# Performance work log

Hardware: AMD Instinct MI355X
Metric: run time of the kernel (lower is better)

Reference implementation:

```python
import jax, jax.numpy as jnp
import numpy as np

B = 65536
N_CHILDREN = 512
HIDDEN = 64


def setup_inputs() -> dict:
    key = jax.random.key(0)
    k1, k2, k3, k4, k5, k6, k7 = jax.random.split(key, 7)
    x_cpm = jax.random.normal(k1, (B, N_CHILDREN), dtype=jnp.float32)
    x_cons = jax.random.normal(k2, (B, 1), dtype=jnp.float32)
    # per-child capacities, strictly positive (used as divisor)
    cap = jax.random.uniform(k3, (1, N_CHILDREN), dtype=jnp.float32) + 0.5
    # small MLP params (torch Linear layout: W is (out, in))
    s1 = 1.0 / np.sqrt(N_CHILDREN + 1)
    s2 = 1.0 / np.sqrt(HIDDEN)
    W1 = jax.random.normal(k4, (HIDDEN, N_CHILDREN + 1), dtype=jnp.float32) * s1
    b1 = jax.random.normal(k5, (HIDDEN,), dtype=jnp.float32) * s1
    W2 = jax.random.normal(k6, (N_CHILDREN, HIDDEN), dtype=jnp.float32) * s2
    b2 = jax.random.normal(k7, (N_CHILDREN,), dtype=jnp.float32) * s2
    return {"x_cpm": x_cpm, "x_cons": x_cons, "cap": cap,
            "W1": W1, "b1": b1, "W2": W2, "b2": b2}


def reference(x_cpm, x_cons, cap, W1, b1, W2, b2):
    cap_sum = jnp.sum(cap)  # scalar Cap_sum
    # epsilon: (B, 1) residual of the aggregate constraint
    epsilon = (x_cons * cap_sum - jnp.sum(x_cpm * cap, axis=1, keepdims=True)) / cap_sum
    concat_input = jnp.concatenate([x_cpm, epsilon], axis=1)  # (B, n_l + 1)
    h1 = jax.nn.relu(concat_input @ W1.T + b1)                # (B, 64)
    z = h1 @ W2.T + b2                                        # (B, n_l)
    # symmetric activation: tanh then row-normalize by the signed sum
    signed = jnp.tanh(z)
    h = signed / jnp.sum(signed, axis=1, keepdims=True)
    # reconcile
    x_c = (x_cpm * cap + h * epsilon * cap_sum) / cap
    return x_c
```

## Files before the change

kernel.cpp:

```cpp
#include <hip/hip_runtime.h>
#include <hip/hip_fp16.h>
#include <math.h>

#define THREADS 256
#define RPB 32
#define NBLK (65536 / RPB)

#define WS_W1    0
#define WS_W1_CH 3072
#define WS_W2    (16 * WS_W1_CH)
#define WS_W2_CH 8192
#define WS_W1L   (WS_W2 + 4 * WS_W2_CH)

#define OFF_W    0
#define SZ_W     32768
#define W1BUF_B  12288
#define OFF_T    (OFF_W + SZ_W)
#define SZ_T     (RPB * 516 * 2)
#define OFF_H1   (OFF_T + SZ_T)
#define SZ_H1    (RPB * 68 * 4)
#define OFF_CI   (OFF_H1 + SZ_H1)
#define SZ_CI    2048
#define OFF_EPS  (OFF_CI + SZ_CI)
#define OFF_EPSC (OFF_EPS + 128)
#define OFF_RS   (OFF_EPSC + 128)
#define SMEM_BYTES (OFF_RS + 128)

__device__ __forceinline__ float fast_tanh(float z) {
    float e = __expf(2.0f * z);
    return fmaf(-2.0f, __builtin_amdgcn_rcpf(e + 1.0f), 1.0f);
}

__global__ __launch_bounds__(256) void prep_kernel(
    const float* __restrict__ W1, const float* __restrict__ W2,
    float* __restrict__ ws)
{
    int tid = blockIdx.x * 256 + threadIdx.x;
    {
        int it = tid >> 11;
        int rem = tid & 2047;
        int jj = rem >> 6, c = rem & 63;
        ws[WS_W1 + it * WS_W1_CH + jj * 68 + c] = W1[c * 513 + it * 32 + jj];
    }
    {
        int j = tid & 3, kf4 = (tid >> 2) & 15, n = (tid >> 6) & 127, ch = tid >> 13;
        int swz = kf4 ^ ((9 * (n >> 2) + (n & 3)) & 15);
        ws[WS_W2 + ch * WS_W2_CH + n * 64 + swz * 4 + j] = W2[tid];
    }
    if (tid < 64) ws[WS_W1L + tid] = W1[tid * 513 + 512];
}

__global__ __launch_bounds__(THREADS, 2) void fused_rgu(
    const float* __restrict__ x, const float* __restrict__ xcons,
    const float* __restrict__ cap, const float* __restrict__ b1,
    const float* __restrict__ b2, const float* __restrict__ ws,
    float* __restrict__ out)
{
    extern __shared__ __align__(16) char smem[];
    float*          s_w    = (float*)(smem + OFF_W);
    unsigned short* s_t    = (unsigned short*)(smem + OFF_T);
    float*          s_h1   = (float*)(smem + OFF_H1);
    float*          s_ci   = (float*)(smem + OFF_CI);
    float*          s_eps  = (float*)(smem + OFF_EPS);
    float*          s_epsC = (float*)(smem + OFF_EPSC);
    float*          s_rs   = (float*)(smem + OFF_RS);

    const int t    = threadIdx.x;
    const int lane = t & 63;
    const int wv   = t >> 6;
    const long r0  = (long)blockIdx.x * RPB;

    {
        const float4* src = (const float4*)(ws + WS_W1);
        float4* dst = (float4*)(smem + OFF_W);
        dst[t] = src[t]; dst[t + 256] = src[t + 256]; dst[t + 512] = src[t + 512];
    }

    float4 capA = *(const float4*)(cap + 4 * lane);
    float4 capB = *(const float4*)(cap + 256 + 4 * lane);
    {
        float c0 = cap[t], c1 = cap[t + 256];
        s_ci[t] = 1.0f / c0; s_ci[t + 256] = 1.0f / c1;
    }
    float capSum;
    {
        float p = capA.x + capA.y + capA.z + capA.w
                + capB.x + capB.y + capB.z + capB.w;
        #pragma unroll
        for (int m = 1; m < 64; m <<= 1) p += __shfl_xor(p, m, 64);
        capSum = p;
    }
    const float invCapSum = 1.0f / capSum;

    #pragma unroll
    for (int rr = 0; rr < 8; ++rr) {
        int r = wv * 8 + rr;
        const float* xr = x + (r0 + r) * 512;
        float4 xA = *(const float4*)(xr + 4 * lane);
        float4 xB = *(const float4*)(xr + 256 + 4 * lane);
        float d = fmaf(xA.x, capA.x, fmaf(xA.y, capA.y,
                  fmaf(xA.z, capA.z, fmaf(xA.w, capA.w,
                  fmaf(xB.x, capB.x, fmaf(xB.y, capB.y,
                  fmaf(xB.z, capB.z, xB.w * capB.w)))))));
        #pragma unroll
        for (int m = 1; m < 64; m <<= 1) d += __shfl_xor(d, m, 64);
        if (lane == 0) {
            float epsC = fmaf(xcons[r0 + r], capSum, -d);
            s_epsC[r] = epsC;
            s_eps[r]  = epsC * invCapSum;
        }
    }
    __syncthreads();

    const int rg = t >> 4;
    const int cg = t & 15;
    float acc0[4] = {0.f, 0.f, 0.f, 0.f};
    float acc1[4] = {0.f, 0.f, 0.f, 0.f};
    {
        const float* xg0 = x + (r0 + 2 * rg) * 512;
        const float* xg1 = xg0 + 512;
        for (int it = 0; it < 16; ++it) {
            const int b = it & 1;
            if (it < 15) {
                const float4* src = (const float4*)(ws + WS_W1 + (it + 1) * WS_W1_CH);
                float4* dst = (float4*)(smem + OFF_W + (b ^ 1) * W1BUF_B);
                dst[t] = src[t]; dst[t + 256] = src[t + 256]; dst[t + 512] = src[t + 512];
            }
            const float* w = (const float*)(smem + OFF_W + b * W1BUF_B);
            const int k0 = it * 32;
            #pragma unroll
            for (int j4 = 0; j4 < 8; ++j4) {
                float4 xv0 = *(const float4*)(xg0 + k0 + j4 * 4);
                float4 xv1 = *(const float4*)(xg1 + k0 + j4 * 4);
                const float* wb = &w[(j4 * 4) * 68 + 4 * cg];
                float wr[4][4];
                #pragma unroll
                for (int dj = 0; dj < 4; ++dj) {
                    float4 w4 = *(const float4*)(wb + dj * 68);
                    wr[dj][0] = w4.x; wr[dj][1] = w4.y; wr[dj][2] = w4.z; wr[dj][3] = w4.w;
                }
                #pragma unroll
                for (int m = 0; m < 4; ++m) {
                    acc0[m] = fmaf(xv0.x, wr[0][m], fmaf(xv0.y, wr[1][m],
                              fmaf(xv0.z, wr[2][m], fmaf(xv0.w, wr[3][m], acc0[m]))));
                    acc1[m] = fmaf(xv1.x, wr[0][m], fmaf(xv1.y, wr[1][m],
                              fmaf(xv1.z, wr[2][m], fmaf(xv1.w, wr[3][m], acc1[m]))));
                }
            }
            __syncthreads();
        }
        float4 b1v = *(const float4*)(b1 + 4 * cg);
        float4 wl  = *(const float4*)(ws + WS_W1L + 4 * cg);
        #pragma unroll
        for (int i = 0; i < 2; ++i) {
            float e = s_eps[2 * rg + i];
            const float* a = i ? acc1 : acc0;
            float4 h;
            h.x = fmaxf(a[0] + fmaf(e, wl.x, b1v.x), 0.f);
            h.y = fmaxf(a[1] + fmaf(e, wl.y, b1v.y), 0.f);
            h.z = fmaxf(a[2] + fmaf(e, wl.z, b1v.z), 0.f);
            h.w = fmaxf(a[3] + fmaf(e, wl.w, b1v.w), 0.f);
            *(float4*)&s_h1[(2 * rg + i) * 68 + 4 * cg] = h;
        }
    }

    const int ng  = t & 31;
    const int rg2 = t >> 5;
    float rsum[4] = {0.f, 0.f, 0.f, 0.f};
    for (int ch = 0; ch < 4; ++ch) {
        __syncthreads();
        {
            const float4* src = (const float4*)(ws + WS_W2 + ch * WS_W2_CH);
            float4* dst = (float4*)(smem + OFF_W);
            #pragma unroll
            for (int e8 = 0; e8 < 8; ++e8) dst[e8 * 256 + t] = src[e8 * 256 + t];
        }
        __syncthreads();
        const int n0 = ch * 128;
        float4 b2v = *(const float4*)(b2 + n0 + 4 * ng);
        float za[4][4];
        #pragma unroll
        for (int i = 0; i < 4; ++i) {
            za[i][0] = b2v.x; za[i][1] = b2v.y; za[i][2] = b2v.z; za[i][3] = b2v.w;
        }
        #pragma unroll
        for (int kf4 = 0; kf4 < 16; ++kf4) {
            float hr[4][4];
            #pragma unroll
            for (int i = 0; i < 4; ++i) {
                float4 h = *(const float4*)&s_h1[(rg2 * 4 + i) * 68 + kf4 * 4];
                hr[i][0] = h.x; hr[i][1] = h.y; hr[i][2] = h.z; hr[i][3] = h.w;
            }
            float wr2[4][4];
            #pragma unroll
            for (int m = 0; m < 4; ++m) {
                int nl = 4 * ng + m;
                int swz = kf4 ^ ((9 * ng + m) & 15);
                float4 w = *(const float4*)&s_w[nl * 64 + swz * 4];
                wr2[m][0] = w.x; wr2[m][1] = w.y; wr2[m][2] = w.z; wr2[m][3] = w.w;
            }
            #pragma unroll
            for (int i = 0; i < 4; ++i)
                #pragma unroll
                for (int m = 0; m < 4; ++m)
                    za[i][m] = fmaf(hr[i][0], wr2[m][0], fmaf(hr[i][1], wr2[m][1],
                               fmaf(hr[i][2], wr2[m][2], fmaf(hr[i][3], wr2[m][3], za[i][m]))));
        }
        #pragma unroll
        for (int i = 0; i < 4; ++i) {
            int r = rg2 * 4 + i;
            float t0 = fast_tanh(za[i][0]);
            float t1 = fast_tanh(za[i][1]);
            float t2 = fast_tanh(za[i][2]);
            float t3 = fast_tanh(za[i][3]);
            rsum[i] += (t0 + t1) + (t2 + t3);
            ushort4 tv4;
            tv4.x = __half_as_ushort(__float2half(t0));
            tv4.y = __half_as_ushort(__float2half(t1));
            tv4.z = __half_as_ushort(__float2half(t2));
            tv4.w = __half_as_ushort(__float2half(t3));
            *(ushort4*)&s_t[r * 516 + n0 + 4 * ng] = tv4;
        }
    }
    #pragma unroll
    for (int i = 0; i < 4; ++i) {
        float s = rsum[i];
        #pragma unroll
        for (int msk = 1; msk < 32; msk <<= 1) s += __shfl_xor(s, msk, 64);
        if (ng == 0) {
            int r = rg2 * 4 + i;
            s_rs[r] = s_epsC[r] / s;
        }
    }
    __syncthreads();

    {
        const int rr  = t >> 7;
        const int col = (t & 127) * 4;
        #pragma unroll 4
        for (int q = 0; q < 16; ++q) {
            int r = q * 2 + rr;
            float rs = s_rs[r];
            float4 xv = *(const float4*)(x + (r0 + r) * 512 + col);
            ushort4 tv4 = *(const ushort4*)&s_t[r * 516 + col];
            float4 ci = *(const float4*)&s_ci[col];
            float4 o;
            o.x = fmaf(__half2float(__ushort_as_half(tv4.x)), rs * ci.x, xv.x);
            o.y = fmaf(__half2float(__ushort_as_half(tv4.y)), rs * ci.y, xv.y);
            o.z = fmaf(__half2float(__ushort_as_half(tv4.z)), rs * ci.z, xv.z);
            o.w = fmaf(__half2float(__ushort_as_half(tv4.w)), rs * ci.w, xv.w);
            *(float4*)(out + (r0 + r) * 512 + col) = o;
        }
    }
}

extern "C" void kernel_launch(void* const* d_in, const int* in_sizes, int n_in,
                              void* d_out, int out_size, void* d_ws, size_t ws_size,
                              hipStream_t stream) {
    const float* x     = (const float*)d_in[0];
    const float* xcons = (const float*)d_in[1];
    const float* cap   = (const float*)d_in[2];
    const float* W1    = (const float*)d_in[3];
    const float* b1    = (const float*)d_in[4];
    const float* W2    = (const float*)d_in[5];
    const float* b2    = (const float*)d_in[6];
    float* out         = (float*)d_out;
    float* ws          = (float*)d_ws;

    (void)in_sizes; (void)n_in; (void)out_size; (void)ws_size;

    prep_kernel<<<128, 256, 0, stream>>>(W1, W2, ws);

    hipFuncSetAttribute((const void*)fused_rgu,
                        hipFuncAttributeMaxDynamicSharedMemorySize, SMEM_BYTES);
    fused_rgu<<<NBLK, THREADS, SMEM_BYTES, stream>>>(
        x, xcons, cap, b1, b2, ws, out);
}
```

Baseline: 444.3 us.

## Keep tanh results in registers instead of LDS and raise occupancy

Packed fp16 tanh outputs now stay in per-thread registers (32 uints) rather than being staged through a shared-memory tile, and the row-sum reciprocal is used directly after the wave shuffle reduction. This removes the s_t and s_rs LDS buffers along with a barrier and the LDS round trip. The smaller LDS footprint plus launch bounds raised to 3 blocks per CU aim for higher occupancy. The cost is more register pressure under the tighter register cap, and the final x/out accesses now follow the GEMM thread mapping (32 threads per row, 16B each, four 512B segments per row) instead of the previous fully contiguous row sweep.

```diff
diff --git a/kernel.cpp b/kernel.cpp
--- a/kernel.cpp
+++ b/kernel.cpp
@@ -15,16 +15,13 @@
 #define OFF_W    0
 #define SZ_W     32768
 #define W1BUF_B  12288
-#define OFF_T    (OFF_W + SZ_W)
-#define SZ_T     (RPB * 516 * 2)
-#define OFF_H1   (OFF_T + SZ_T)
+#define OFF_H1   (OFF_W + SZ_W)
 #define SZ_H1    (RPB * 68 * 4)
 #define OFF_CI   (OFF_H1 + SZ_H1)
 #define SZ_CI    2048
 #define OFF_EPS  (OFF_CI + SZ_CI)
 #define OFF_EPSC (OFF_EPS + 128)
-#define OFF_RS   (OFF_EPSC + 128)
-#define SMEM_BYTES (OFF_RS + 128)
+#define SMEM_BYTES (OFF_EPSC + 128)
 
 __device__ __forceinline__ float fast_tanh(float z) {
     float e = __expf(2.0f * z);
@@ -50,7 +47,7 @@
     if (tid < 64) ws[WS_W1L + tid] = W1[tid * 513 + 512];
 }
 
-__global__ __launch_bounds__(THREADS, 2) void fused_rgu(
+__global__ __launch_bounds__(THREADS, 3) void fused_rgu(
     const float* __restrict__ x, const float* __restrict__ xcons,
     const float* __restrict__ cap, const float* __restrict__ b1,
     const float* __restrict__ b2, const float* __restrict__ ws,
@@ -58,12 +55,10 @@
 {
     extern __shared__ __align__(16) char smem[];
     float*          s_w    = (float*)(smem + OFF_W);
-    unsigned short* s_t    = (unsigned short*)(smem + OFF_T);
     float*          s_h1   = (float*)(smem + OFF_H1);
     float*          s_ci   = (float*)(smem + OFF_CI);
     float*          s_eps  = (float*)(smem + OFF_EPS);
     float*          s_epsC = (float*)(smem + OFF_EPSC);
-    float*          s_rs   = (float*)(smem + OFF_RS);
 
     const int t    = threadIdx.x;
     const int lane = t & 63;
@@ -167,6 +162,8 @@
     const int ng  = t & 31;
     const int rg2 = t >> 5;
     float rsum[4] = {0.f, 0.f, 0.f, 0.f};
+    unsigned tp[4][4][2];
+    #pragma unroll
     for (int ch = 0; ch < 4; ++ch) {
         __syncthreads();
         {
@@ -208,48 +205,46 @@
         }
         #pragma unroll
         for (int i = 0; i < 4; ++i) {
-            int r = rg2 * 4 + i;
             float t0 = fast_tanh(za[i][0]);
             float t1 = fast_tanh(za[i][1]);
             float t2 = fast_tanh(za[i][2]);
             float t3 = fast_tanh(za[i][3]);
             rsum[i] += (t0 + t1) + (t2 + t3);
-            ushort4 tv4;
-            tv4.x = __half_as_ushort(__float2half(t0));
-            tv4.y = __half_as_ushort(__float2half(t1));
-            tv4.z = __half_as_ushort(__float2half(t2));
-            tv4.w = __half_as_ushort(__float2half(t3));
-            *(ushort4*)&s_t[r * 516 + n0 + 4 * ng] = tv4;
-        }
-    }
+            __half2 h01 = __floats2half2_rn(t0, t1);
+            __half2 h23 = __floats2half2_rn(t2, t3);
+            tp[ch][i][0] = *(unsigned*)&h01;
+            tp[ch][i][1] = *(unsigned*)&h23;
+        }
+    }
+
+    float rs[4];
     #pragma unroll
     for (int i = 0; i < 4; ++i) {
         float s = rsum[i];
         #pragma unroll
         for (int msk = 1; msk < 32; msk <<= 1) s += __shfl_xor(s, msk, 64);
-        if (ng == 0) {
-            int r = rg2 * 4 + i;
-            s_rs[r] = s_epsC[r] / s;
-        }
-    }
-    __syncthreads();
-
-    {
-        const int rr  = t >> 7;
-        const int col = (t & 127) * 4;
-        #pragma unroll 4
-        for (int q = 0; q < 16; ++q) {
-            int r = q * 2 + rr;
-            float rs = s_rs[r];
-            float4 xv = *(const float4*)(x + (r0 + r) * 512 + col);
-            ushort4 tv4 = *(const ushort4*)&s_t[r * 516 + col];
-            float4 ci = *(const float4*)&s_ci[col];
+        rs[i] = s_epsC[rg2 * 4 + i] / s;
+    }
+
+    #pragma unroll
+    for (int ch = 0; ch < 4; ++ch) {
+        const int c = ch * 128 + 4 * ng;
+        float4 ci = *(const float4*)&s_ci[c];
+        #pragma unroll
+        for (int i = 0; i < 4; ++i) {
+            const int r = rg2 * 4 + i;
+            float4 xv = *(const float4*)(x + (r0 + r) * 512 + c);
+            __half2 h01 = *(__half2*)&tp[ch][i][0];
+            __half2 h23 = *(__half2*)&tp[ch][i][1];
+            float2 f01 = __half22float2(h01);
+            float2 f23 = __half22float2(h23);
+            float ri = rs[i];
             float4 o;
-            o.x = fmaf(__half2float(__ushort_as_half(tv4.x)), rs * ci.x, xv.x);
-            o.y = fmaf(__half2float(__ushort_as_half(tv4.y)), rs * ci.y, xv.y);
-            o.z = fmaf(__half2float(__ushort_as_half(tv4.z)), rs * ci.z, xv.z);
-            o.w = fmaf(__half2float(__ushort_as_half(tv4.w)), rs * ci.w, xv.w);
-            *(float4*)(out + (r0 + r) * 512 + col) = o;
+            o.x = fmaf(f01.x, ri * ci.x, xv.x);
+            o.y = fmaf(f01.y, ri * ci.y, xv.y);
+            o.z = fmaf(f23.x, ri * ci.z, xv.z);
+            o.w = fmaf(f23.y, ri * ci.w, xv.w);
+            *(float4*)(out + (r0 + r) * 512 + c) = o;
         }
     }
 }
```

New measurement: 389.3 us. 12.4% less time.
